# Kernel tuning notes

Hardware: AMD Instinct MI355X
Metric: run time of the kernel (lower is better)

## Reference

```python
import jax, jax.numpy as jnp
import numpy as np

N = 20000       # nodes
E = 320000      # edges (without self-loops)
D_IN = 256
HID = 64        # per-head channels, layer 1
HEADS = 4
D_OUT = 256
EPS = 1e-5      # LayerNorm eps
SLOPE = 0.2     # LeakyReLU negative slope (PyG GATConv default)


def setup_inputs() -> dict:
    key = jax.random.key(0)
    ks = jax.random.split(key, 10)
    def glorot(k, shape):
        fan_in, fan_out = shape[0], int(np.prod(shape[1:]))
        s = np.sqrt(2.0 / (fan_in + fan_out)).astype(np.float32)
        return jax.random.normal(k, shape, dtype=jnp.float32) * s
    x = jax.random.normal(ks[0], (N, D_IN), dtype=jnp.float32)
    edge_index = jax.random.randint(ks[1], (2, E), 0, N, dtype=jnp.int64)
    return {
        "x": x,
        "edge_index": edge_index,
        # layer 1: GATConv(D_IN, HID, heads=4, concat=True)
        "W1": glorot(ks[2], (D_IN, HEADS * HID)),
        "a1_src": glorot(ks[3], (HEADS, HID)),
        "a1_dst": glorot(ks[4], (HEADS, HID)),
        "b1": jnp.zeros((HEADS * HID,), jnp.float32),
        # LayerNorm(HEADS*HID)
        "ln_g": jnp.ones((HEADS * HID,), jnp.float32),
        "ln_b": jnp.zeros((HEADS * HID,), jnp.float32),
        # layer 2: GATConv(HEADS*HID, D_OUT, heads=1, concat=False)
        "W2": glorot(ks[5], (HEADS * HID, D_OUT)),
        "a2_src": glorot(ks[6], (1, D_OUT)),
        "a2_dst": glorot(ks[7], (1, D_OUT)),
        "b2": jnp.zeros((D_OUT,), jnp.float32),
    }


def _gat(x, src, dst, W, a_src, a_dst, b, heads, ch, concat):
    """PyG-style GATConv (self-loops already appended to src/dst)."""
    n = x.shape[0]
    h = (x @ W).reshape(n, heads, ch)                      # [n,H,C]
    es = (h * a_src).sum(-1)                               # [n,H] src logits
    ed = (h * a_dst).sum(-1)                               # [n,H] dst logits
    e = jax.nn.leaky_relu(es[src] + ed[dst], SLOPE)        # [Etot,H]
    # softmax over incoming edges of each dst node (stable)
    m = jax.ops.segment_max(e, dst, num_segments=n)
    w = jnp.exp(e - m[dst])
    den = jax.ops.segment_sum(w, dst, num_segments=n)
    alpha = w / den[dst]                                   # [Etot,H]
    msg = h[src] * alpha[:, :, None]                       # [Etot,H,C]
    out = jax.ops.segment_sum(msg, dst, num_segments=n)    # [n,H,C]
    out = out.reshape(n, heads * ch) if concat else out.mean(axis=1)
    return out + b


def _layernorm(x, g, b):
    mu = x.mean(-1, keepdims=True)
    v = ((x - mu) ** 2).mean(-1, keepdims=True)
    return (x - mu) * jax.lax.rsqrt(v + EPS) * g + b


def reference(x, edge_index, W1, a1_src, a1_dst, b1, ln_g, ln_b, W2, a2_src, a2_dst, b2):
    loops = jnp.arange(N, dtype=edge_index.dtype)
    src = jnp.concatenate([edge_index[0], loops])
    dst = jnp.concatenate([edge_index[1], loops])
    h = _gat(x, src, dst, W1, a1_src, a1_dst, b1, HEADS, HID, True)
    h = jax.nn.relu(_layernorm(h, ln_g, ln_b))             # dropout is identity in eval
    out = _gat(h, src, dst, W2, a2_src, a2_dst, b2, 1, D_OUT, False)
    return out
```

## Files before the change

kernel.cpp:

```cpp
#include <hip/hip_runtime.h>
#include <hip/hip_bf16.h>
#include <math.h>

#define N_NODES 20000
#define N_EDGES 320000
#define N_ETOT  (N_EDGES + N_NODES)
#define SLOPE 0.2f
#define LN_EPS 1e-5f
#define CNT_BLOCKS 1329

typedef __attribute__((ext_vector_type(8))) short short8v;
typedef __attribute__((ext_vector_type(4))) float f32x4;

__device__ __forceinline__ float lrelu(float x) { return x > 0.f ? x : SLOPE * x; }

__device__ __forceinline__ float rlf(float v, int l) {
  return __uint_as_float(__builtin_amdgcn_readlane(__float_as_uint(v), l));
}
__device__ __forceinline__ int rli(int v, int l) { return __builtin_amdgcn_readlane(v, l); }

__device__ __forceinline__ unsigned short f2bf(float f) {
  __hip_bfloat16 h = __float2bfloat16(f);
  return *reinterpret_cast<unsigned short*>(&h);
}
__device__ __forceinline__ float bf2f(unsigned short u) {
  return __uint_as_float(((unsigned int)u) << 16);
}

__global__ __launch_bounds__(256) void k_count_prep(const int* __restrict__ ei, int* __restrict__ cnt,
                                                    const float* __restrict__ W1, const float* __restrict__ W2,
                                                    unsigned short* __restrict__ P1, unsigned short* __restrict__ P2) {
  int b = blockIdx.x, tid = threadIdx.x;
  if (b < CNT_BLOCKS) {
    int i = b * 256 + tid;
    if (i < N_ETOT) {
      int d = (i < N_EDGES) ? ei[N_EDGES + i] : (i - N_EDGES);
      atomicAdd(&cnt[d], 1);
    }
  } else {
    int e = (b - CNT_BLOCKS) * 256 + tid;
    int j = e & 7, lane = (e >> 3) & 63, nf = (e >> 9) & 15, ks = (e >> 13) & 7;
    int col = nf * 16 + (lane & 15);
    int k = ks * 32 + (lane >> 4) * 8 + j;
    P1[e] = f2bf(W1[k * 256 + col]);
    P2[e] = f2bf(W2[k * 256 + col]);
  }
}

__device__ __forceinline__ int blockScan512(int val, int tid, int* ldsw, int* total) {
  int lane = tid & 63, w = tid >> 6;
  int incl = val;
#pragma unroll
  for (int d = 1; d < 64; d <<= 1) { int t = __shfl_up(incl, d); if (lane >= d) incl += t; }
  if (lane == 63) ldsw[w] = incl;
  __syncthreads();
  if (w == 0 && lane < 8) {
    int s = ldsw[lane];
#pragma unroll
    for (int d = 1; d < 8; d <<= 1) { int t = __shfl_up(s, d); if (lane >= d) s += t; }
    ldsw[lane] = s;
  }
  __syncthreads();
  if (w > 0) incl += ldsw[w - 1];
  *total = ldsw[7];
  return incl;
}

__global__ __launch_bounds__(512) void k_scanA(const int* __restrict__ cnt, int* __restrict__ off,
                                               int* __restrict__ bsum) {
  __shared__ int ldsw[8];
  int tid = threadIdx.x, b = blockIdx.x;
  int g = b * 512 + tid;
  int val = (g < N_NODES) ? cnt[g] : 0;
  int tot;
  int incl = blockScan512(val, tid, ldsw, &tot);
  if (g < N_NODES) off[g + 1] = incl;
  if (tid == 0) bsum[b] = tot;
}

__global__ __launch_bounds__(512) void k_scanB(int* __restrict__ off, const int* __restrict__ bsum,
                                               int* __restrict__ cnt) {
  __shared__ int sbase;
  int tid = threadIdx.x, b = blockIdx.x;
  if (tid < 64) {
    int v = (tid < 40) ? bsum[tid] : 0;
    int inc = v;
#pragma unroll
    for (int d = 1; d < 64; d <<= 1) { int t = __shfl_up(inc, d); if (tid >= d) inc += t; }
    int base = (b == 0) ? 0 : rli(inc, b - 1);
    if (tid == 0) sbase = base;
  }
  __syncthreads();
  int base = sbase;
  int g = b * 512 + tid;
  if (g < N_NODES) {
    off[g + 1] += base;
    cnt[g] = 0;
  }
  if (g == 0) off[0] = 0;
}

__global__ __launch_bounds__(256) void k_scatter(const int* __restrict__ ei, const int* __restrict__ off,
                                                 int* __restrict__ cursor, int* __restrict__ srcs) {
  int i = blockIdx.x * 256 + threadIdx.x;
  if (i >= N_ETOT) return;
  int s, d;
  if (i < N_EDGES) { s = ei[i]; d = ei[N_EDGES + i]; } else { s = i - N_EDGES; d = s; }
  int pos = off[d] + atomicAdd(&cursor[d], 1);
  srcs[pos] = s;
}

template <int A_BF16, int HEADS>
__global__ __launch_bounds__(256) void k_gemm(const void* __restrict__ Av,
                                              const unsigned short* __restrict__ Wp,
                                              const float* __restrict__ asrc,
                                              const float* __restrict__ adst,
                                              unsigned short* __restrict__ C,
                                              float* __restrict__ es, float* __restrict__ ed) {
  int gwave = blockIdx.x * 4 + (threadIdx.x >> 6);
  if (gwave >= 1250) return;
  int lane = threadIdx.x & 63;
  int r = lane & 15, kg = lane >> 4;
  int rbase = gwave * 16;

  f32x4 acc[16];
#pragma unroll
  for (int i = 0; i < 16; ++i) acc[i] = (f32x4){0.f, 0.f, 0.f, 0.f};

  const float* Af = (const float*)Av;
  const unsigned short* Ab = (const unsigned short*)Av;

#pragma unroll
  for (int ks = 0; ks < 8; ++ks) {
    int koff = ks * 32 + kg * 8;
    short8v a;
    if (A_BF16) {
      int4 raw = *reinterpret_cast<const int4*>(&Ab[(size_t)(rbase + r) * 256 + koff]);
      a = __builtin_bit_cast(short8v, raw);
    } else {
      float4 lo = *reinterpret_cast<const float4*>(&Af[(size_t)(rbase + r) * 256 + koff]);
      float4 hi = *reinterpret_cast<const float4*>(&Af[(size_t)(rbase + r) * 256 + koff + 4]);
      a[0] = (short)f2bf(lo.x); a[1] = (short)f2bf(lo.y); a[2] = (short)f2bf(lo.z); a[3] = (short)f2bf(lo.w);
      a[4] = (short)f2bf(hi.x); a[5] = (short)f2bf(hi.y); a[6] = (short)f2bf(hi.z); a[7] = (short)f2bf(hi.w);
    }
#pragma unroll
    for (int nf = 0; nf < 16; ++nf) {
      int4 braw = *reinterpret_cast<const int4*>(&Wp[(size_t)(ks * 16 + nf) * 512 + lane * 8]);
      short8v bfr = __builtin_bit_cast(short8v, braw);
      acc[nf] = __builtin_amdgcn_mfma_f32_16x16x32_bf16(a, bfr, acc[nf], 0, 0, 0);
    }
  }

#pragma unroll
  for (int nf = 0; nf < 16; ++nf) {
#pragma unroll
    for (int q = 0; q < 4; ++q) {
      C[(size_t)(rbase + kg * 4 + q) * 256 + nf * 16 + r] = f2bf(acc[nf][q]);
    }
  }

  float as_v[16], ad_v[16];
#pragma unroll
  for (int nf = 0; nf < 16; ++nf) {
    as_v[nf] = asrc[nf * 16 + r];
    ad_v[nf] = adst[nf * 16 + r];
  }
  if (HEADS == 4) {
#pragma unroll
    for (int q = 0; q < 4; ++q) {
      float hs[4], hd[4];
#pragma unroll
      for (int h = 0; h < 4; ++h) {
        hs[h] = 0.f; hd[h] = 0.f;
#pragma unroll
        for (int t = 0; t < 4; ++t) {
          int nf = h * 4 + t;
          hs[h] = fmaf(acc[nf][q], as_v[nf], hs[h]);
          hd[h] = fmaf(acc[nf][q], ad_v[nf], hd[h]);
        }
#pragma unroll
        for (int s = 1; s < 16; s <<= 1) {
          hs[h] += __shfl_xor(hs[h], s);
          hd[h] += __shfl_xor(hd[h], s);
        }
      }
      if (r == 0) {
        int row = rbase + kg * 4 + q;
#pragma unroll
        for (int h = 0; h < 4; ++h) {
          es[row * 4 + h] = hs[h];
          ed[row * 4 + h] = hd[h];
        }
      }
    }
  } else {
#pragma unroll
    for (int q = 0; q < 4; ++q) {
      float s0 = 0.f, d0 = 0.f;
#pragma unroll
      for (int nf = 0; nf < 16; ++nf) {
        s0 = fmaf(acc[nf][q], as_v[nf], s0);
        d0 = fmaf(acc[nf][q], ad_v[nf], d0);
      }
#pragma unroll
      for (int s = 1; s < 16; s <<= 1) {
        s0 += __shfl_xor(s0, s);
        d0 += __shfl_xor(d0, s);
      }
      if (r == 0) {
        int row = rbase + kg * 4 + q;
        es[row] = s0;
        ed[row] = d0;
      }
    }
  }
}

__global__ __launch_bounds__(256) void k_gat1_ln(const unsigned short* __restrict__ h1,
                                                 const float* __restrict__ es, const float* __restrict__ ed,
                                                 const int* __restrict__ off, const int* __restrict__ srcs,
                                                 const float* __restrict__ b1, const float* __restrict__ lng,
                                                 const float* __restrict__ lnb, unsigned short* __restrict__ hmid) {
  int n = (blockIdx.x * 256 + threadIdx.x) >> 6;
  if (n >= N_NODES) return;
  int lane = threadIdx.x & 63;
  int myh = lane >> 4;
  int beg = off[n], end = off[n + 1], deg = end - beg;
  float4 edv = *reinterpret_cast<const float4*>(&ed[n * 4]);
  float ax = 0.f, ay = 0.f, az = 0.f, aw = 0.f;
  float invden;

  if (deg <= 64) {
    int sv = 0;
    float e0 = -1e30f, e1 = -1e30f, e2 = -1e30f, e3 = -1e30f;
    bool valid = lane < deg;
    if (valid) {
      sv = srcs[beg + lane];
      float4 esv = *reinterpret_cast<const float4*>(&es[sv * 4]);
      e0 = lrelu(esv.x + edv.x); e1 = lrelu(esv.y + edv.y);
      e2 = lrelu(esv.z + edv.z); e3 = lrelu(esv.w + edv.w);
    }
    float m0 = e0, m1 = e1, m2 = e2, m3 = e3;
#pragma unroll
    for (int s = 1; s < 64; s <<= 1) {
      m0 = fmaxf(m0, __shfl_xor(m0, s)); m1 = fmaxf(m1, __shfl_xor(m1, s));
      m2 = fmaxf(m2, __shfl_xor(m2, s)); m3 = fmaxf(m3, __shfl_xor(m3, s));
    }
    float w0 = valid ? __expf(e0 - m0) : 0.f;
    float w1 = valid ? __expf(e1 - m1) : 0.f;
    float w2 = valid ? __expf(e2 - m2) : 0.f;
    float w3 = valid ? __expf(e3 - m3) : 0.f;
    float d0 = w0, d1 = w1, d2 = w2, d3 = w3;
#pragma unroll
    for (int s = 1; s < 64; s <<= 1) {
      d0 += __shfl_xor(d0, s); d1 += __shfl_xor(d1, s);
      d2 += __shfl_xor(d2, s); d3 += __shfl_xor(d3, s);
    }
    float den = (myh == 0) ? d0 : (myh == 1) ? d1 : (myh == 2) ? d2 : d3;
    invden = 1.f / den;

    int j = 0;
    for (; j + 4 <= deg; j += 4) {
      int s0 = rli(sv, j), s1 = rli(sv, j + 1), s2 = rli(sv, j + 2), s3 = rli(sv, j + 3);
      ushort4 v0 = *reinterpret_cast<const ushort4*>(&h1[(size_t)s0 * 256 + lane * 4]);
      ushort4 v1 = *reinterpret_cast<const ushort4*>(&h1[(size_t)s1 * 256 + lane * 4]);
      ushort4 v2 = *reinterpret_cast<const ushort4*>(&h1[(size_t)s2 * 256 + lane * 4]);
      ushort4 v3 = *reinterpret_cast<const ushort4*>(&h1[(size_t)s3 * 256 + lane * 4]);
#pragma unroll
      for (int q = 0; q < 4; ++q) {
        int jj = j + q;
        float w0j = rlf(w0, jj), w1j = rlf(w1, jj), w2j = rlf(w2, jj), w3j = rlf(w3, jj);
        float wj = (myh == 0) ? w0j : (myh == 1) ? w1j : (myh == 2) ? w2j : w3j;
        ushort4 v = (q == 0) ? v0 : (q == 1) ? v1 : (q == 2) ? v2 : v3;
        ax = fmaf(wj, bf2f(v.x), ax); ay = fmaf(wj, bf2f(v.y), ay);
        az = fmaf(wj, bf2f(v.z), az); aw = fmaf(wj, bf2f(v.w), aw);
      }
    }
    for (; j < deg; ++j) {
      int sj = rli(sv, j);
      float w0j = rlf(w0, j), w1j = rlf(w1, j), w2j = rlf(w2, j), w3j = rlf(w3, j);
      float wj = (myh == 0) ? w0j : (myh == 1) ? w1j : (myh == 2) ? w2j : w3j;
      ushort4 v = *reinterpret_cast<const ushort4*>(&h1[(size_t)sj * 256 + lane * 4]);
      ax = fmaf(wj, bf2f(v.x), ax); ay = fmaf(wj, bf2f(v.y), ay);
      az = fmaf(wj, bf2f(v.z), az); aw = fmaf(wj, bf2f(v.w), aw);
    }
  } else {
    float m0 = -1e30f, m1 = -1e30f, m2 = -1e30f, m3 = -1e30f;
    for (int j = beg + lane; j < end; j += 64) {
      int s = srcs[j];
      float4 esv = *reinterpret_cast<const float4*>(&es[s * 4]);
      m0 = fmaxf(m0, lrelu(esv.x + edv.x)); m1 = fmaxf(m1, lrelu(esv.y + edv.y));
      m2 = fmaxf(m2, lrelu(esv.z + edv.z)); m3 = fmaxf(m3, lrelu(esv.w + edv.w));
    }
#pragma unroll
    for (int s = 1; s < 64; s <<= 1) {
      m0 = fmaxf(m0, __shfl_xor(m0, s)); m1 = fmaxf(m1, __shfl_xor(m1, s));
      m2 = fmaxf(m2, __shfl_xor(m2, s)); m3 = fmaxf(m3, __shfl_xor(m3, s));
    }
    float edh = (myh == 0) ? edv.x : (myh == 1) ? edv.y : (myh == 2) ? edv.z : edv.w;
    float mh = (myh == 0) ? m0 : (myh == 1) ? m1 : (myh == 2) ? m2 : m3;
    float den = 0.f;
    for (int j = beg; j < end; ++j) {
      int s = srcs[j];
      float e = lrelu(es[s * 4 + myh] + edh);
      float w = __expf(e - mh);
      den += w;
      ushort4 v = *reinterpret_cast<const ushort4*>(&h1[(size_t)s * 256 + lane * 4]);
      ax = fmaf(w, bf2f(v.x), ax); ay = fmaf(w, bf2f(v.y), ay);
      az = fmaf(w, bf2f(v.z), az); aw = fmaf(w, bf2f(v.w), aw);
    }
    invden = 1.f / den;
  }

  float4 bb = *reinterpret_cast<const float4*>(&b1[lane * 4]);
  float vx = ax * invden + bb.x, vy = ay * invden + bb.y;
  float vz = az * invden + bb.z, vw = aw * invden + bb.w;
  float sum = vx + vy + vz + vw;
  float sq = vx * vx + vy * vy + vz * vz + vw * vw;
#pragma unroll
  for (int s = 1; s < 64; s <<= 1) { sum += __shfl_xor(sum, s); sq += __shfl_xor(sq, s); }
  float mu = sum * (1.f / 256.f);
  float var = sq * (1.f / 256.f) - mu * mu;
  float rstd = rsqrtf(var + LN_EPS);
  float4 g = *reinterpret_cast<const float4*>(&lng[lane * 4]);
  float4 lb = *reinterpret_cast<const float4*>(&lnb[lane * 4]);
  ushort4 o;
  o.x = f2bf(fmaxf(0.f, (vx - mu) * rstd * g.x + lb.x));
  o.y = f2bf(fmaxf(0.f, (vy - mu) * rstd * g.y + lb.y));
  o.z = f2bf(fmaxf(0.f, (vz - mu) * rstd * g.z + lb.z));
  o.w = f2bf(fmaxf(0.f, (vw - mu) * rstd * g.w + lb.w));
  *reinterpret_cast<ushort4*>(&hmid[(size_t)n * 256 + lane * 4]) = o;
}

__global__ __launch_bounds__(256) void k_gat2(const unsigned short* __restrict__ h2,
                                              const float* __restrict__ es, const float* __restrict__ ed,
                                              const int* __restrict__ off, const int* __restrict__ srcs,
                                              const float* __restrict__ b2, float* __restrict__ out) {
  int n = (blockIdx.x * 256 + threadIdx.x) >> 6;
  if (n >= N_NODES) return;
  int lane = threadIdx.x & 63;
  int beg = off[n], end = off[n + 1], deg = end - beg;
  float edn = ed[n];
  float ax = 0.f, ay = 0.f, az = 0.f, aw = 0.f;
  float invden;

  if (deg <= 64) {
    int sv = 0;
    float e = -1e30f;
    bool valid = lane < deg;
    if (valid) {
      sv = srcs[beg + lane];
      e = lrelu(es[sv] + edn);
    }
    float m = e;
#pragma unroll
    for (int s = 1; s < 64; s <<= 1) m = fmaxf(m, __shfl_xor(m, s));
    float wv = valid ? __expf(e - m) : 0.f;
    float den = wv;
#pragma unroll
    for (int s = 1; s < 64; s <<= 1) den += __shfl_xor(den, s);
    invden = 1.f / den;

    int j = 0;
    for (; j + 4 <= deg; j += 4) {
      int s0 = rli(sv, j), s1 = rli(sv, j + 1), s2 = rli(sv, j + 2), s3 = rli(sv, j + 3);
      ushort4 v0 = *reinterpret_cast<const ushort4*>(&h2[(size_t)s0 * 256 + lane * 4]);
      ushort4 v1 = *reinterpret_cast<const ushort4*>(&h2[(size_t)s1 * 256 + lane * 4]);
      ushort4 v2 = *reinterpret_cast<const ushort4*>(&h2[(size_t)s2 * 256 + lane * 4]);
      ushort4 v3 = *reinterpret_cast<const ushort4*>(&h2[(size_t)s3 * 256 + lane * 4]);
      float wj0 = rlf(wv, j), wj1 = rlf(wv, j + 1), wj2 = rlf(wv, j + 2), wj3 = rlf(wv, j + 3);
      ax = fmaf(wj0, bf2f(v0.x), ax); ay = fmaf(wj0, bf2f(v0.y), ay);
      az = fmaf(wj0, bf2f(v0.z), az); aw = fmaf(wj0, bf2f(v0.w), aw);
      ax = fmaf(wj1, bf2f(v1.x), ax); ay = fmaf(wj1, bf2f(v1.y), ay);
      az = fmaf(wj1, bf2f(v1.z), az); aw = fmaf(wj1, bf2f(v1.w), aw);
      ax = fmaf(wj2, bf2f(v2.x), ax); ay = fmaf(wj2, bf2f(v2.y), ay);
      az = fmaf(wj2, bf2f(v2.z), az); aw = fmaf(wj2, bf2f(v2.w), aw);
      ax = fmaf(wj3, bf2f(v3.x), ax); ay = fmaf(wj3, bf2f(v3.y), ay);
      az = fmaf(wj3, bf2f(v3.z), az); aw = fmaf(wj3, bf2f(v3.w), aw);
    }
    for (; j < deg; ++j) {
      int sj = rli(sv, j);
      float wj = rlf(wv, j);
      ushort4 v = *reinterpret_cast<const ushort4*>(&h2[(size_t)sj * 256 + lane * 4]);
      ax = fmaf(wj, bf2f(v.x), ax); ay = fmaf(wj, bf2f(v.y), ay);
      az = fmaf(wj, bf2f(v.z), az); aw = fmaf(wj, bf2f(v.w), aw);
    }
  } else {
    float m = -1e30f;
    for (int j = beg + lane; j < end; j += 64) m = fmaxf(m, lrelu(es[srcs[j]] + edn));
#pragma unroll
    for (int s = 1; s < 64; s <<= 1) m = fmaxf(m, __shfl_xor(m, s));
    float den = 0.f;
    for (int j = beg; j < end; ++j) {
      int s = srcs[j];
      float w = __expf(lrelu(es[s] + edn) - m);
      den += w;
      ushort4 v = *reinterpret_cast<const ushort4*>(&h2[(size_t)s * 256 + lane * 4]);
      ax = fmaf(w, bf2f(v.x), ax); ay = fmaf(w, bf2f(v.y), ay);
      az = fmaf(w, bf2f(v.z), az); aw = fmaf(w, bf2f(v.w), aw);
    }
    invden = 1.f / den;
  }

  float4 bb = *reinterpret_cast<const float4*>(&b2[lane * 4]);
  float4 o = make_float4(ax * invden + bb.x, ay * invden + bb.y, az * invden + bb.z, aw * invden + bb.w);
  *reinterpret_cast<float4*>(&out[(size_t)n * 256 + lane * 4]) = o;
}

extern "C" void kernel_launch(void* const* d_in, const int* in_sizes, int n_in,
                              void* d_out, int out_size, void* d_ws, size_t ws_size,
                              hipStream_t stream) {
  (void)in_sizes; (void)n_in; (void)out_size; (void)ws_size;
  const float* x   = (const float*)d_in[0];
  const int*   ei  = (const int*)d_in[1];
  const float* W1  = (const float*)d_in[2];
  const float* a1s = (const float*)d_in[3];
  const float* a1d = (const float*)d_in[4];
  const float* b1  = (const float*)d_in[5];
  const float* lng = (const float*)d_in[6];
  const float* lnb = (const float*)d_in[7];
  const float* W2  = (const float*)d_in[8];
  const float* a2s = (const float*)d_in[9];
  const float* a2d = (const float*)d_in[10];
  const float* b2  = (const float*)d_in[11];
  float* out = (float*)d_out;

  char* ws = (char*)d_ws;
  unsigned short* h1b   = (unsigned short*)(ws + 0);
  unsigned short* hmidb = (unsigned short*)(ws + 10240000);
  unsigned short* h2b   = (unsigned short*)(ws + 20480000);
  unsigned short* Wp1   = (unsigned short*)(ws + 30720000);
  unsigned short* Wp2   = (unsigned short*)(ws + 30851072);
  float* es1 = (float*)(ws + 30982144);
  float* ed1 = (float*)(ws + 31302144);
  float* es2 = (float*)(ws + 31622144);
  float* ed2 = (float*)(ws + 31702144);
  int*   off = (int*)(ws + 31782144);
  int*   cnt = (int*)(ws + 31862148);
  int*   srcs = (int*)(ws + 31942148);
  int*   bsum = (int*)(ws + 33302160);

  hipMemsetAsync(cnt, 0, N_NODES * sizeof(int), stream);
  k_count_prep<<<CNT_BLOCKS + 256, 256, 0, stream>>>(ei, cnt, W1, W2, Wp1, Wp2);
  k_scanA<<<40, 512, 0, stream>>>(cnt, off, bsum);
  k_scanB<<<40, 512, 0, stream>>>(off, bsum, cnt);
  k_scatter<<<CNT_BLOCKS, 256, 0, stream>>>(ei, off, cnt, srcs);

  k_gemm<0, 4><<<313, 256, 0, stream>>>((const void*)x, Wp1, a1s, a1d, h1b, es1, ed1);
  k_gat1_ln<<<(N_NODES * 64) / 256, 256, 0, stream>>>(h1b, es1, ed1, off, srcs, b1, lng, lnb, hmidb);

  k_gemm<1, 1><<<313, 256, 0, stream>>>((const void*)hmidb, Wp2, a2s, a2d, h2b, es2, ed2);
  k_gat2<<<(N_NODES * 64) / 256, 256, 0, stream>>>(h2b, es2, ed2, off, srcs, b2, out);
}
```

Measured before the change: 217.3 us.

## Fuse GAT1 aggregation with layer-2 GEMM and merge edge count with GEMM1

```diff
diff --git a/kernel.cpp b/kernel.cpp
--- a/kernel.cpp
+++ b/kernel.cpp
@@ -27,9 +27,30 @@
   return __uint_as_float(((unsigned int)u) << 16);
 }
 
-__global__ __launch_bounds__(256) void k_count_prep(const int* __restrict__ ei, int* __restrict__ cnt,
-                                                    const float* __restrict__ W1, const float* __restrict__ W2,
-                                                    unsigned short* __restrict__ P1, unsigned short* __restrict__ P2) {
+__global__ __launch_bounds__(256) void k_init(const float* __restrict__ W1, const float* __restrict__ W2,
+                                              unsigned short* __restrict__ P1, unsigned short* __restrict__ P2,
+                                              int* __restrict__ cnt) {
+  int b = blockIdx.x, t = threadIdx.x;
+  if (b < 256) {
+    int e = b * 256 + t;
+    int j = e & 7, lane = (e >> 3) & 63, nf = (e >> 9) & 15, ks = (e >> 13) & 7;
+    int col = nf * 16 + (lane & 15);
+    int k = ks * 32 + (lane >> 4) * 8 + j;
+    P1[e] = f2bf(W1[k * 256 + col]);
+    P2[e] = f2bf(W2[k * 256 + col]);
+  } else {
+    int i = (b - 256) * 256 + t;
+    if (i < N_NODES) cnt[i] = 0;
+  }
+}
+
+__global__ __launch_bounds__(256) void k_count_gemm1(const int* __restrict__ ei, int* __restrict__ cnt,
+                                                     const float* __restrict__ x,
+                                                     const unsigned short* __restrict__ Wp,
+                                                     const float* __restrict__ asrc,
+                                                     const float* __restrict__ adst,
+                                                     unsigned short* __restrict__ C,
+                                                     float* __restrict__ es, float* __restrict__ ed) {
   int b = blockIdx.x, tid = threadIdx.x;
   if (b < CNT_BLOCKS) {
     int i = b * 256 + tid;
@@ -37,13 +58,73 @@
       int d = (i < N_EDGES) ? ei[N_EDGES + i] : (i - N_EDGES);
       atomicAdd(&cnt[d], 1);
     }
-  } else {
-    int e = (b - CNT_BLOCKS) * 256 + tid;
-    int j = e & 7, lane = (e >> 3) & 63, nf = (e >> 9) & 15, ks = (e >> 13) & 7;
-    int col = nf * 16 + (lane & 15);
-    int k = ks * 32 + (lane >> 4) * 8 + j;
-    P1[e] = f2bf(W1[k * 256 + col]);
-    P2[e] = f2bf(W2[k * 256 + col]);
+    return;
+  }
+  int gwave = (b - CNT_BLOCKS) * 4 + (tid >> 6);
+  if (gwave >= 1250) return;
+  int lane = tid & 63;
+  int r = lane & 15, kg = lane >> 4;
+  int rbase = gwave * 16;
+
+  f32x4 acc[16];
+#pragma unroll
+  for (int i = 0; i < 16; ++i) acc[i] = (f32x4){0.f, 0.f, 0.f, 0.f};
+
+#pragma unroll
+  for (int ks = 0; ks < 8; ++ks) {
+    int koff = ks * 32 + kg * 8;
+    float4 lo = *reinterpret_cast<const float4*>(&x[(size_t)(rbase + r) * 256 + koff]);
+    float4 hi = *reinterpret_cast<const float4*>(&x[(size_t)(rbase + r) * 256 + koff + 4]);
+    short8v a;
+    a[0] = (short)f2bf(lo.x); a[1] = (short)f2bf(lo.y); a[2] = (short)f2bf(lo.z); a[3] = (short)f2bf(lo.w);
+    a[4] = (short)f2bf(hi.x); a[5] = (short)f2bf(hi.y); a[6] = (short)f2bf(hi.z); a[7] = (short)f2bf(hi.w);
+#pragma unroll
+    for (int nf = 0; nf < 16; ++nf) {
+      int4 braw = *reinterpret_cast<const int4*>(&Wp[(size_t)(ks * 16 + nf) * 512 + lane * 8]);
+      short8v bfr = __builtin_bit_cast(short8v, braw);
+      acc[nf] = __builtin_amdgcn_mfma_f32_16x16x32_bf16(a, bfr, acc[nf], 0, 0, 0);
+    }
+  }
+
+#pragma unroll
+  for (int nf = 0; nf < 16; ++nf) {
+#pragma unroll
+    for (int q = 0; q < 4; ++q)
+      C[(size_t)(rbase + kg * 4 + q) * 256 + nf * 16 + r] = f2bf(acc[nf][q]);
+  }
+
+  float as_v[16], ad_v[16];
+#pragma unroll
+  for (int nf = 0; nf < 16; ++nf) {
+    as_v[nf] = asrc[nf * 16 + r];
+    ad_v[nf] = adst[nf * 16 + r];
+  }
+#pragma unroll
+  for (int q = 0; q < 4; ++q) {
+    float hs[4], hd[4];
+#pragma unroll
+    for (int h = 0; h < 4; ++h) {
+      hs[h] = 0.f; hd[h] = 0.f;
+#pragma unroll
+      for (int t = 0; t < 4; ++t) {
+        int nf = h * 4 + t;
+        hs[h] = fmaf(acc[nf][q], as_v[nf], hs[h]);
+        hd[h] = fmaf(acc[nf][q], ad_v[nf], hd[h]);
+      }
+#pragma unroll
+      for (int s = 1; s < 16; s <<= 1) {
+        hs[h] += __shfl_xor(hs[h], s);
+        hd[h] += __shfl_xor(hd[h], s);
+      }
+    }
+    if (r == 0) {
+      int row = rbase + kg * 4 + q;
+#pragma unroll
+      for (int h = 0; h < 4; ++h) {
+        es[row * 4 + h] = hs[h];
+        ed[row * 4 + h] = hd[h];
+      }
+    }
   }
 }
 
@@ -110,226 +191,189 @@
   srcs[pos] = s;
 }
 
-template <int A_BF16, int HEADS>
-__global__ __launch_bounds__(256) void k_gemm(const void* __restrict__ Av,
-                                              const unsigned short* __restrict__ Wp,
-                                              const float* __restrict__ asrc,
-                                              const float* __restrict__ adst,
-                                              unsigned short* __restrict__ C,
-                                              float* __restrict__ es, float* __restrict__ ed) {
-  int gwave = blockIdx.x * 4 + (threadIdx.x >> 6);
-  if (gwave >= 1250) return;
-  int lane = threadIdx.x & 63;
+__global__ __launch_bounds__(256) void k_gat1_gemm2(const unsigned short* __restrict__ h1,
+                                                    const float* __restrict__ es, const float* __restrict__ ed,
+                                                    const int* __restrict__ off, const int* __restrict__ srcs,
+                                                    const float* __restrict__ b1, const float* __restrict__ lng,
+                                                    const float* __restrict__ lnb,
+                                                    const unsigned short* __restrict__ Wp,
+                                                    const float* __restrict__ a2s, const float* __restrict__ a2d,
+                                                    unsigned short* __restrict__ h2b,
+                                                    float* __restrict__ es2, float* __restrict__ ed2) {
+  __shared__ char hm[16 * 512];
+  __shared__ float esp[4][16], edp[4][16];
+  int tid = threadIdx.x;
+  int w = tid >> 6, lane = tid & 63;
+  int myh = lane >> 4;
+  int nbase = blockIdx.x * 16;
+
+  for (int i = 0; i < 4; ++i) {
+    int lrow = w * 4 + i;
+    int n = nbase + lrow;
+    int beg = off[n], end = off[n + 1], deg = end - beg;
+    float4 edv = *reinterpret_cast<const float4*>(&ed[n * 4]);
+    float ax = 0.f, ay = 0.f, az = 0.f, aw = 0.f;
+    float invden;
+
+    if (deg <= 64) {
+      int sv = 0;
+      float e0 = -1e30f, e1 = -1e30f, e2 = -1e30f, e3 = -1e30f;
+      bool valid = lane < deg;
+      if (valid) {
+        sv = srcs[beg + lane];
+        float4 esv = *reinterpret_cast<const float4*>(&es[sv * 4]);
+        e0 = lrelu(esv.x + edv.x); e1 = lrelu(esv.y + edv.y);
+        e2 = lrelu(esv.z + edv.z); e3 = lrelu(esv.w + edv.w);
+      }
+      float m0 = e0, m1 = e1, m2 = e2, m3 = e3;
+#pragma unroll
+      for (int s = 1; s < 64; s <<= 1) {
+        m0 = fmaxf(m0, __shfl_xor(m0, s)); m1 = fmaxf(m1, __shfl_xor(m1, s));
+        m2 = fmaxf(m2, __shfl_xor(m2, s)); m3 = fmaxf(m3, __shfl_xor(m3, s));
+      }
+      float w0 = valid ? __expf(e0 - m0) : 0.f;
+      float w1 = valid ? __expf(e1 - m1) : 0.f;
+      float w2 = valid ? __expf(e2 - m2) : 0.f;
+      float w3 = valid ? __expf(e3 - m3) : 0.f;
+      float d0 = w0, d1 = w1, d2 = w2, d3 = w3;
+#pragma unroll
+      for (int s = 1; s < 64; s <<= 1) {
+        d0 += __shfl_xor(d0, s); d1 += __shfl_xor(d1, s);
+        d2 += __shfl_xor(d2, s); d3 += __shfl_xor(d3, s);
+      }
+      float den = (myh == 0) ? d0 : (myh == 1) ? d1 : (myh == 2) ? d2 : d3;
+      invden = 1.f / den;
+
+      int j = 0;
+      for (; j + 4 <= deg; j += 4) {
+        int s0 = rli(sv, j), s1 = rli(sv, j + 1), s2 = rli(sv, j + 2), s3 = rli(sv, j + 3);
+        ushort4 v0 = *reinterpret_cast<const ushort4*>(&h1[(size_t)s0 * 256 + lane * 4]);
+        ushort4 v1 = *reinterpret_cast<const ushort4*>(&h1[(size_t)s1 * 256 + lane * 4]);
+        ushort4 v2 = *reinterpret_cast<const ushort4*>(&h1[(size_t)s2 * 256 + lane * 4]);
+        ushort4 v3 = *reinterpret_cast<const ushort4*>(&h1[(size_t)s3 * 256 + lane * 4]);
+#pragma unroll
+        for (int q = 0; q < 4; ++q) {
+          int jj = j + q;
+          float w0j = rlf(w0, jj), w1j = rlf(w1, jj), w2j = rlf(w2, jj), w3j = rlf(w3, jj);
+          float wj = (myh == 0) ? w0j : (myh == 1) ? w1j : (myh == 2) ? w2j : w3j;
+          ushort4 v = (q == 0) ? v0 : (q == 1) ? v1 : (q == 2) ? v2 : v3;
+          ax = fmaf(wj, bf2f(v.x), ax); ay = fmaf(wj, bf2f(v.y), ay);
+          az = fmaf(wj, bf2f(v.z), az); aw = fmaf(wj, bf2f(v.w), aw);
+        }
+      }
+      for (; j < deg; ++j) {
+        int sj = rli(sv, j);
+        float w0j = rlf(w0, j), w1j = rlf(w1, j), w2j = rlf(w2, j), w3j = rlf(w3, j);
+        float wj = (myh == 0) ? w0j : (myh == 1) ? w1j : (myh == 2) ? w2j : w3j;
+        ushort4 v = *reinterpret_cast<const ushort4*>(&h1[(size_t)sj * 256 + lane * 4]);
+        ax = fmaf(wj, bf2f(v.x), ax); ay = fmaf(wj, bf2f(v.y), ay);
+        az = fmaf(wj, bf2f(v.z), az); aw = fmaf(wj, bf2f(v.w), aw);
+      }
+    } else {
+      float m0 = -1e30f, m1 = -1e30f, m2 = -1e30f, m3 = -1e30f;
+      for (int j = beg + lane; j < end; j += 64) {
+        int s = srcs[j];
+        float4 esv = *reinterpret_cast<const float4*>(&es[s * 4]);
+        m0 = fmaxf(m0, lrelu(esv.x + edv.x)); m1 = fmaxf(m1, lrelu(esv.y + edv.y));
+        m2 = fmaxf(m2, lrelu(esv.z + edv.z)); m3 = fmaxf(m3, lrelu(esv.w + edv.w));
+      }
+#pragma unroll
+      for (int s = 1; s < 64; s <<= 1) {
+        m0 = fmaxf(m0, __shfl_xor(m0, s)); m1 = fmaxf(m1, __shfl_xor(m1, s));
+        m2 = fmaxf(m2, __shfl_xor(m2, s)); m3 = fmaxf(m3, __shfl_xor(m3, s));
+      }
+      float edh = (myh == 0) ? edv.x : (myh == 1) ? edv.y : (myh == 2) ? edv.z : edv.w;
+      float mh = (myh == 0) ? m0 : (myh == 1) ? m1 : (myh == 2) ? m2 : m3;
+      float den = 0.f;
+      for (int j = beg; j < end; ++j) {
+        int s = srcs[j];
+        float e = lrelu(es[s * 4 + myh] + edh);
+        float wj = __expf(e - mh);
+        den += wj;
+        ushort4 v = *reinterpret_cast<const ushort4*>(&h1[(size_t)s * 256 + lane * 4]);
+        ax = fmaf(wj, bf2f(v.x), ax); ay = fmaf(wj, bf2f(v.y), ay);
+        az = fmaf(wj, bf2f(v.z), az); aw = fmaf(wj, bf2f(v.w), aw);
+      }
+      invden = 1.f / den;
+    }
+
+    float4 bb = *reinterpret_cast<const float4*>(&b1[lane * 4]);
+    float vx = ax * invden + bb.x, vy = ay * invden + bb.y;
+    float vz = az * invden + bb.z, vw = aw * invden + bb.w;
+    float sum = vx + vy + vz + vw;
+    float sq = vx * vx + vy * vy + vz * vz + vw * vw;
+#pragma unroll
+    for (int s = 1; s < 64; s <<= 1) { sum += __shfl_xor(sum, s); sq += __shfl_xor(sq, s); }
+    float mu = sum * (1.f / 256.f);
+    float var = sq * (1.f / 256.f) - mu * mu;
+    float rstd = rsqrtf(var + LN_EPS);
+    float4 g = *reinterpret_cast<const float4*>(&lng[lane * 4]);
+    float4 lb = *reinterpret_cast<const float4*>(&lnb[lane * 4]);
+    ushort4 o;
+    o.x = f2bf(fmaxf(0.f, (vx - mu) * rstd * g.x + lb.x));
+    o.y = f2bf(fmaxf(0.f, (vy - mu) * rstd * g.y + lb.y));
+    o.z = f2bf(fmaxf(0.f, (vz - mu) * rstd * g.z + lb.z));
+    o.w = f2bf(fmaxf(0.f, (vw - mu) * rstd * g.w + lb.w));
+    *reinterpret_cast<ushort4*>(&hm[lrow * 512 + ((lane * 8 + lrow * 64) & 511)]) = o;
+  }
+  __syncthreads();
+
   int r = lane & 15, kg = lane >> 4;
-  int rbase = gwave * 16;
-
-  f32x4 acc[16];
-#pragma unroll
-  for (int i = 0; i < 16; ++i) acc[i] = (f32x4){0.f, 0.f, 0.f, 0.f};
-
-  const float* Af = (const float*)Av;
-  const unsigned short* Ab = (const unsigned short*)Av;
+  f32x4 acc[4];
+#pragma unroll
+  for (int i = 0; i < 4; ++i) acc[i] = (f32x4){0.f, 0.f, 0.f, 0.f};
 
 #pragma unroll
   for (int ks = 0; ks < 8; ++ks) {
-    int koff = ks * 32 + kg * 8;
-    short8v a;
-    if (A_BF16) {
-      int4 raw = *reinterpret_cast<const int4*>(&Ab[(size_t)(rbase + r) * 256 + koff]);
-      a = __builtin_bit_cast(short8v, raw);
-    } else {
-      float4 lo = *reinterpret_cast<const float4*>(&Af[(size_t)(rbase + r) * 256 + koff]);
-      float4 hi = *reinterpret_cast<const float4*>(&Af[(size_t)(rbase + r) * 256 + koff + 4]);
-      a[0] = (short)f2bf(lo.x); a[1] = (short)f2bf(lo.y); a[2] = (short)f2bf(lo.z); a[3] = (short)f2bf(lo.w);
-      a[4] = (short)f2bf(hi.x); a[5] = (short)f2bf(hi.y); a[6] = (short)f2bf(hi.z); a[7] = (short)f2bf(hi.w);
-    }
-#pragma unroll
-    for (int nf = 0; nf < 16; ++nf) {
+    int4 araw = *reinterpret_cast<const int4*>(
+        &hm[r * 512 + (((ks * 64 + kg * 16) + r * 64) & 511)]);
+    short8v a = __builtin_bit_cast(short8v, araw);
+#pragma unroll
+    for (int nf2 = 0; nf2 < 4; ++nf2) {
+      int nf = w * 4 + nf2;
       int4 braw = *reinterpret_cast<const int4*>(&Wp[(size_t)(ks * 16 + nf) * 512 + lane * 8]);
       short8v bfr = __builtin_bit_cast(short8v, braw);
-      acc[nf] = __builtin_amdgcn_mfma_f32_16x16x32_bf16(a, bfr, acc[nf], 0, 0, 0);
-    }
-  }
-
-#pragma unroll
-  for (int nf = 0; nf < 16; ++nf) {
-#pragma unroll
-    for (int q = 0; q < 4; ++q) {
-      C[(size_t)(rbase + kg * 4 + q) * 256 + nf * 16 + r] = f2bf(acc[nf][q]);
-    }
-  }
-
-  float as_v[16], ad_v[16];
-#pragma unroll
-  for (int nf = 0; nf < 16; ++nf) {
-    as_v[nf] = asrc[nf * 16 + r];
-    ad_v[nf] = adst[nf * 16 + r];
-  }
-  if (HEADS == 4) {
-#pragma unroll
-    for (int q = 0; q < 4; ++q) {
-      float hs[4], hd[4];
-#pragma unroll
-      for (int h = 0; h < 4; ++h) {
-        hs[h] = 0.f; hd[h] = 0.f;
-#pragma unroll
-        for (int t = 0; t < 4; ++t) {
-          int nf = h * 4 + t;
-          hs[h] = fmaf(acc[nf][q], as_v[nf], hs[h]);
-          hd[h] = fmaf(acc[nf][q], ad_v[nf], hd[h]);
-        }
-#pragma unroll
-        for (int s = 1; s < 16; s <<= 1) {
-          hs[h] += __shfl_xor(hs[h], s);
-          hd[h] += __shfl_xor(hd[h], s);
-        }
-      }
-      if (r == 0) {
-        int row = rbase + kg * 4 + q;
-#pragma unroll
-        for (int h = 0; h < 4; ++h) {
-          es[row * 4 + h] = hs[h];
-          ed[row * 4 + h] = hd[h];
-        }
-      }
-    }
-  } else {
-#pragma unroll
-    for (int q = 0; q < 4; ++q) {
-      float s0 = 0.f, d0 = 0.f;
-#pragma unroll
-      for (int nf = 0; nf < 16; ++nf) {
-        s0 = fmaf(acc[nf][q], as_v[nf], s0);
-        d0 = fmaf(acc[nf][q], ad_v[nf], d0);
-      }
-#pragma unroll
-      for (int s = 1; s < 16; s <<= 1) {
-        s0 += __shfl_xor(s0, s);
-        d0 += __shfl_xor(d0, s);
-      }
-      if (r == 0) {
-        int row = rbase + kg * 4 + q;
-        es[row] = s0;
-        ed[row] = d0;
-      }
-    }
-  }
-}
-
-__global__ __launch_bounds__(256) void k_gat1_ln(const unsigned short* __restrict__ h1,
-                                                 const float* __restrict__ es, const float* __restrict__ ed,
-                                                 const int* __restrict__ off, const int* __restrict__ srcs,
-                                                 const float* __restrict__ b1, const float* __restrict__ lng,
-                                                 const float* __restrict__ lnb, unsigned short* __restrict__ hmid) {
-  int n = (blockIdx.x * 256 + threadIdx.x) >> 6;
-  if (n >= N_NODES) return;
-  int lane = threadIdx.x & 63;
-  int myh = lane >> 4;
-  int beg = off[n], end = off[n + 1], deg = end - beg;
-  float4 edv = *reinterpret_cast<const float4*>(&ed[n * 4]);
-  float ax = 0.f, ay = 0.f, az = 0.f, aw = 0.f;
-  float invden;
-
-  if (deg <= 64) {
-    int sv = 0;
-    float e0 = -1e30f, e1 = -1e30f, e2 = -1e30f, e3 = -1e30f;
-    bool valid = lane < deg;
-    if (valid) {
-      sv = srcs[beg + lane];
-      float4 esv = *reinterpret_cast<const float4*>(&es[sv * 4]);
-      e0 = lrelu(esv.x + edv.x); e1 = lrelu(esv.y + edv.y);
-      e2 = lrelu(esv.z + edv.z); e3 = lrelu(esv.w + edv.w);
-    }
-    float m0 = e0, m1 = e1, m2 = e2, m3 = e3;
-#pragma unroll
-    for (int s = 1; s < 64; s <<= 1) {
-      m0 = fmaxf(m0, __shfl_xor(m0, s)); m1 = fmaxf(m1, __shfl_xor(m1, s));
-      m2 = fmaxf(m2, __shfl_xor(m2, s)); m3 = fmaxf(m3, __shfl_xor(m3, s));
-    }
-    float w0 = valid ? __expf(e0 - m0) : 0.f;
-    float w1 = valid ? __expf(e1 - m1) : 0.f;
-    float w2 = valid ? __expf(e2 - m2) : 0.f;
-    float w3 = valid ? __expf(e3 - m3) : 0.f;
-    float d0 = w0, d1 = w1, d2 = w2, d3 = w3;
-#pragma unroll
-    for (int s = 1; s < 64; s <<= 1) {
-      d0 += __shfl_xor(d0, s); d1 += __shfl_xor(d1, s);
-      d2 += __shfl_xor(d2, s); d3 += __shfl_xor(d3, s);
-    }
-    float den = (myh == 0) ? d0 : (myh == 1) ? d1 : (myh == 2) ? d2 : d3;
-    invden = 1.f / den;
-
-    int j = 0;
-    for (; j + 4 <= deg; j += 4) {
-      int s0 = rli(sv, j), s1 = rli(sv, j + 1), s2 = rli(sv, j + 2), s3 = rli(sv, j + 3);
-      ushort4 v0 = *reinterpret_cast<const ushort4*>(&h1[(size_t)s0 * 256 + lane * 4]);
-      ushort4 v1 = *reinterpret_cast<const ushort4*>(&h1[(size_t)s1 * 256 + lane * 4]);
-      ushort4 v2 = *reinterpret_cast<const ushort4*>(&h1[(size_t)s2 * 256 + lane * 4]);
-      ushort4 v3 = *reinterpret_cast<const ushort4*>(&h1[(size_t)s3 * 256 + lane * 4]);
-#pragma unroll
-      for (int q = 0; q < 4; ++q) {
-        int jj = j + q;
-        float w0j = rlf(w0, jj), w1j = rlf(w1, jj), w2j = rlf(w2, jj), w3j = rlf(w3, jj);
-        float wj = (myh == 0) ? w0j : (myh == 1) ? w1j : (myh == 2) ? w2j : w3j;
-        ushort4 v = (q == 0) ? v0 : (q == 1) ? v1 : (q == 2) ? v2 : v3;
-        ax = fmaf(wj, bf2f(v.x), ax); ay = fmaf(wj, bf2f(v.y), ay);
-        az = fmaf(wj, bf2f(v.z), az); aw = fmaf(wj, bf2f(v.w), aw);
-      }
-    }
-    for (; j < deg; ++j) {
-      int sj = rli(sv, j);
-      float w0j = rlf(w0, j), w1j = rlf(w1, j), w2j = rlf(w2, j), w3j = rlf(w3, j);
-      float wj = (myh == 0) ? w0j : (myh == 1) ? w1j : (myh == 2) ? w2j : w3j;
-      ushort4 v = *reinterpret_cast<const ushort4*>(&h1[(size_t)sj * 256 + lane * 4]);
-      ax = fmaf(wj, bf2f(v.x), ax); ay = fmaf(wj, bf2f(v.y), ay);
-      az = fmaf(wj, bf2f(v.z), az); aw = fmaf(wj, bf2f(v.w), aw);
-    }
-  } else {
-    float m0 = -1e30f, m1 = -1e30f, m2 = -1e30f, m3 = -1e30f;
-    for (int j = beg + lane; j < end; j += 64) {
-      int s = srcs[j];
-      float4 esv = *reinterpret_cast<const float4*>(&es[s * 4]);
-      m0 = fmaxf(m0, lrelu(esv.x + edv.x)); m1 = fmaxf(m1, lrelu(esv.y + edv.y));
-      m2 = fmaxf(m2, lrelu(esv.z + edv.z)); m3 = fmaxf(m3, lrelu(esv.w + edv.w));
-    }
-#pragma unroll
-    for (int s = 1; s < 64; s <<= 1) {
-      m0 = fmaxf(m0, __shfl_xor(m0, s)); m1 = fmaxf(m1, __shfl_xor(m1, s));
-      m2 = fmaxf(m2, __shfl_xor(m2, s)); m3 = fmaxf(m3, __shfl_xor(m3, s));
-    }
-    float edh = (myh == 0) ? edv.x : (myh == 1) ? edv.y : (myh == 2) ? edv.z : edv.w;
-    float mh = (myh == 0) ? m0 : (myh == 1) ? m1 : (myh == 2) ? m2 : m3;
-    float den = 0.f;
-    for (int j = beg; j < end; ++j) {
-      int s = srcs[j];
-      float e = lrelu(es[s * 4 + myh] + edh);
-      float w = __expf(e - mh);
-      den += w;
-      ushort4 v = *reinterpret_cast<const ushort4*>(&h1[(size_t)s * 256 + lane * 4]);
-      ax = fmaf(w, bf2f(v.x), ax); ay = fmaf(w, bf2f(v.y), ay);
-      az = fmaf(w, bf2f(v.z), az); aw = fmaf(w, bf2f(v.w), aw);
-    }
-    invden = 1.f / den;
-  }
-
-  float4 bb = *reinterpret_cast<const float4*>(&b1[lane * 4]);
-  float vx = ax * invden + bb.x, vy = ay * invden + bb.y;
-  float vz = az * invden + bb.z, vw = aw * invden + bb.w;
-  float sum = vx + vy + vz + vw;
-  float sq = vx * vx + vy * vy + vz * vz + vw * vw;
-#pragma unroll
-  for (int s = 1; s < 64; s <<= 1) { sum += __shfl_xor(sum, s); sq += __shfl_xor(sq, s); }
-  float mu = sum * (1.f / 256.f);
-  float var = sq * (1.f / 256.f) - mu * mu;
-  float rstd = rsqrtf(var + LN_EPS);
-  float4 g = *reinterpret_cast<const float4*>(&lng[lane * 4]);
-  float4 lb = *reinterpret_cast<const float4*>(&lnb[lane * 4]);
-  ushort4 o;
-  o.x = f2bf(fmaxf(0.f, (vx - mu) * rstd * g.x + lb.x));
-  o.y = f2bf(fmaxf(0.f, (vy - mu) * rstd * g.y + lb.y));
-  o.z = f2bf(fmaxf(0.f, (vz - mu) * rstd * g.z + lb.z));
-  o.w = f2bf(fmaxf(0.f, (vw - mu) * rstd * g.w + lb.w));
-  *reinterpret_cast<ushort4*>(&hmid[(size_t)n * 256 + lane * 4]) = o;
+      acc[nf2] = __builtin_amdgcn_mfma_f32_16x16x32_bf16(a, bfr, acc[nf2], 0, 0, 0);
+    }
+  }
+
+  int rbase = nbase;
+#pragma unroll
+  for (int nf2 = 0; nf2 < 4; ++nf2) {
+#pragma unroll
+    for (int q = 0; q < 4; ++q)
+      h2b[(size_t)(rbase + kg * 4 + q) * 256 + w * 64 + nf2 * 16 + r] = f2bf(acc[nf2][q]);
+  }
+
+  float as_v[4], ad_v[4];
+#pragma unroll
+  for (int nf2 = 0; nf2 < 4; ++nf2) {
+    as_v[nf2] = a2s[w * 64 + nf2 * 16 + r];
+    ad_v[nf2] = a2d[w * 64 + nf2 * 16 + r];
+  }
+#pragma unroll
+  for (int q = 0; q < 4; ++q) {
+    float s0 = 0.f, d0 = 0.f;
+#pragma unroll
+    for (int nf2 = 0; nf2 < 4; ++nf2) {
+      s0 = fmaf(acc[nf2][q], as_v[nf2], s0);
+      d0 = fmaf(acc[nf2][q], ad_v[nf2], d0);
+    }
+#pragma unroll
+    for (int s = 1; s < 16; s <<= 1) {
+      s0 += __shfl_xor(s0, s);
+      d0 += __shfl_xor(d0, s);
+    }
+    if (r == 0) {
+      esp[w][kg * 4 + q] = s0;
+      edp[w][kg * 4 + q] = d0;
+    }
+  }
+  __syncthreads();
+  if (tid < 16) {
+    es2[rbase + tid] = esp[0][tid] + esp[1][tid] + esp[2][tid] + esp[3][tid];
+    ed2[rbase + tid] = edp[0][tid] + edp[1][tid] + edp[2][tid] + edp[3][tid];
+  }
 }
 
 __global__ __launch_bounds__(256) void k_gat2(const unsigned short* __restrict__ h2,
@@ -393,11 +437,11 @@
     float den = 0.f;
     for (int j = beg; j < end; ++j) {
       int s = srcs[j];
-      float w = __expf(lrelu(es[s] + edn) - m);
-      den += w;
+      float wj = __expf(lrelu(es[s] + edn) - m);
+      den += wj;
       ushort4 v = *reinterpret_cast<const ushort4*>(&h2[(size_t)s * 256 + lane * 4]);
-      ax = fmaf(w, bf2f(v.x), ax); ay = fmaf(w, bf2f(v.y), ay);
-      az = fmaf(w, bf2f(v.z), az); aw = fmaf(w, bf2f(v.w), aw);
+      ax = fmaf(wj, bf2f(v.x), ax); ay = fmaf(wj, bf2f(v.y), ay);
+      az = fmaf(wj, bf2f(v.z), az); aw = fmaf(wj, bf2f(v.w), aw);
     }
     invden = 1.f / den;
   }
@@ -426,29 +470,25 @@
   float* out = (float*)d_out;
 
   char* ws = (char*)d_ws;
-  unsigned short* h1b   = (unsigned short*)(ws + 0);
-  unsigned short* hmidb = (unsigned short*)(ws + 10240000);
-  unsigned short* h2b   = (unsigned short*)(ws + 20480000);
-  unsigned short* Wp1   = (unsigned short*)(ws + 30720000);
-  unsigned short* Wp2   = (unsigned short*)(ws + 30851072);
-  float* es1 = (float*)(ws + 30982144);
-  float* ed1 = (float*)(ws + 31302144);
-  float* es2 = (float*)(ws + 31622144);
-  float* ed2 = (float*)(ws + 31702144);
-  int*   off = (int*)(ws + 31782144);
-  int*   cnt = (int*)(ws + 31862148);
-  int*   srcs = (int*)(ws + 31942148);
-  int*   bsum = (int*)(ws + 33302160);
-
-  hipMemsetAsync(cnt, 0, N_NODES * sizeof(int), stream);
-  k_count_prep<<<CNT_BLOCKS + 256, 256, 0, stream>>>(ei, cnt, W1, W2, Wp1, Wp2);
+  unsigned short* h1b = (unsigned short*)(ws + 0);
+  unsigned short* h2b = (unsigned short*)(ws + 10240000);
+  unsigned short* Wp1 = (unsigned short*)(ws + 20480000);
+  unsigned short* Wp2 = (unsigned short*)(ws + 20611072);
+  float* es1 = (float*)(ws + 20742144);
+  float* ed1 = (float*)(ws + 21062144);
+  float* es2 = (float*)(ws + 21382144);
+  float* ed2 = (float*)(ws + 21462144);
+  int*   off = (int*)(ws + 21542144);
+  int*   cnt = (int*)(ws + 21622148);
+  int*   srcs = (int*)(ws + 21702148);
+  int*   bsum = (int*)(ws + 23062160);
+
+  k_init<<<256 + 79, 256, 0, stream>>>(W1, W2, Wp1, Wp2, cnt);
+  k_count_gemm1<<<CNT_BLOCKS + 313, 256, 0, stream>>>(ei, cnt, x, Wp1, a1s, a1d, h1b, es1, ed1);
   k_scanA<<<40, 512, 0, stream>>>(cnt, off, bsum);
   k_scanB<<<40, 512, 0, stream>>>(off, bsum, cnt);
   k_scatter<<<CNT_BLOCKS, 256, 0, stream>>>(ei, off, cnt, srcs);
-
-  k_gemm<0, 4><<<313, 256, 0, stream>>>((const void*)x, Wp1, a1s, a1d, h1b, es1, ed1);
-  k_gat1_ln<<<(N_NODES * 64) / 256, 256, 0, stream>>>(h1b, es1, ed1, off, srcs, b1, lng, lnb, hmidb);
-
-  k_gemm<1, 1><<<313, 256, 0, stream>>>((const void*)hmidb, Wp2, a2s, a2d, h2b, es2, ed2);
+  k_gat1_gemm2<<<1250, 256, 0, stream>>>(h1b, es1, ed1, off, srcs, b1, lng, lnb,
+                                         Wp2, a2s, a2d, h2b, es2, ed2);
   k_gat2<<<(N_NODES * 64) / 256, 256, 0, stream>>>(h2b, es2, ed2, off, srcs, b2, out);
 }
```

Result: faster. 207.4 us (-4.6%).
